# Kernel optimization log

Measured on AMD Instinct MI355X. Metric: run time of the kernel, lower is better.

## Reference

```python
import jax, jax.numpy as jnp
import numpy as np

N = 50000
E = 800000
F_IN = 128
H = 64
C = 10
BN_EPS = 1e-5


def _glorot(key, shape):
    fan_in = shape[0]
    return jax.random.normal(key, shape, dtype=jnp.float32) / jnp.sqrt(jnp.float32(fan_in))


def setup_inputs() -> dict:
    key = jax.random.key(0)
    ks = jax.random.split(key, 16)
    inp = {
        "x": jax.random.normal(ks[0], (N, F_IN), dtype=jnp.float32),
        "edge_index": jax.random.randint(ks[1], (2, E), 0, N, dtype=jnp.int64),
    }
    # GINConv layer params: eps (train_eps=True, init 0), 2-layer MLP, BN affine
    dims = [(F_IN, H), (H, H), (H, H)]
    for i, (din, dout) in enumerate(dims, start=1):
        k1, k2 = jax.random.split(ks[1 + i], 2)
        inp[f"eps{i}"] = jnp.float32(0.0)
        inp[f"w{i}a"] = _glorot(k1, (din, H))
        inp[f"b{i}a"] = jnp.zeros((H,), jnp.float32)
        inp[f"w{i}b"] = _glorot(k2, (H, H))
        inp[f"b{i}b"] = jnp.zeros((H,), jnp.float32)
        inp[f"g{i}"] = jnp.ones((H,), jnp.float32)
        inp[f"be{i}"] = jnp.zeros((H,), jnp.float32)
    inp["lin_w"] = _glorot(ks[10], (H, C))
    inp["lin_b"] = jnp.zeros((C,), jnp.float32)
    return inp


def _gin_conv(x, src, dst, eps, wa, ba, wb, bb, g, be):
    # sum-aggregate neighbor features: scatter-add x[src] into dst rows
    agg = jax.ops.segment_sum(x[src], dst, num_segments=N)
    h = (1.0 + eps) * x + agg
    # MLP: Linear-ReLU-Linear-ReLU-BatchNorm1d (training-mode batch stats)
    h = jax.nn.relu(h @ wa + ba)
    h = jax.nn.relu(h @ wb + bb)
    mean = jnp.mean(h, axis=0)
    var = jnp.var(h, axis=0)
    return (h - mean) * jax.lax.rsqrt(var + BN_EPS) * g + be


def reference(x, edge_index,
              eps1, w1a, b1a, w1b, b1b, g1, be1,
              eps2, w2a, b2a, w2b, b2b, g2, be2,
              eps3, w3a, b3a, w3b, b3b, g3, be3,
              lin_w, lin_b):
    src, dst = edge_index[0], edge_index[1]
    h = jax.nn.relu(_gin_conv(x, src, dst, eps1, w1a, b1a, w1b, b1b, g1, be1))
    h = jax.nn.relu(_gin_conv(h, src, dst, eps2, w2a, b2a, w2b, b2b, g2, be2))
    h = jax.nn.relu(_gin_conv(h, src, dst, eps3, w3a, b3a, w3b, b3b, g3, be3))
    return h @ lin_w + lin_b
```

## Files before the change

kernel.cpp:

```cpp
#include <hip/hip_runtime.h>
#include <hip/hip_fp16.h>

#define NN 50000
#define NGROUP 3125
#define NCHUNK 391
#define CHCAP 3072
#define SLAB 2048
#define BN_EPS 1e-5f

typedef unsigned int uint;
typedef unsigned short ushort;
typedef _Float16 half8 __attribute__((ext_vector_type(8)));
typedef _Float16 half2t __attribute__((ext_vector_type(2)));
typedef float floatx4 __attribute__((ext_vector_type(4)));

__device__ __forceinline__ int aswz(int slot) { return slot ^ ((slot >> 4) & 7); }

__device__ __forceinline__ float h_lo(uint u) {
    return __half2float(__ushort_as_half((ushort)(u & 0xFFFFu)));
}
__device__ __forceinline__ float h_hi(uint u) {
    return __half2float(__ushort_as_half((ushort)(u >> 16)));
}
__device__ __forceinline__ void unpack8(uint4 v, float* f) {
    f[0] = h_lo(v.x); f[1] = h_hi(v.x);
    f[2] = h_lo(v.y); f[3] = h_hi(v.y);
    f[4] = h_lo(v.z); f[5] = h_hi(v.z);
    f[6] = h_lo(v.w); f[7] = h_hi(v.w);
}
__device__ __forceinline__ uint pkadd(uint a, uint b) {
    half2t x = __builtin_bit_cast(half2t, a);
    half2t y = __builtin_bit_cast(half2t, b);
    half2t r = x + y;
    return __builtin_bit_cast(uint, r);
}

__global__ __launch_bounds__(256, 4) void sortA_kernel(
    const int* __restrict__ ei, int* __restrict__ gcur,
    uint* __restrict__ bucket, int E)
{
    __shared__ int s_hist[NCHUNK];
    __shared__ int s_offs[NCHUNK];
    __shared__ int s_cur[NCHUNK];
    __shared__ int s_gb[NCHUNK];
    __shared__ int s_scanA[512], s_scanB[512];
    __shared__ uint s_sorted[SLAB];

    const int tid  = threadIdx.x;
    const int base = blockIdx.x * SLAB;
    const int cnt  = min(SLAB, E - base);

    for (int i = tid; i < NCHUNK; i += 256) s_hist[i] = 0;
    __syncthreads();
    for (int i = tid; i < cnt; i += 256) {
        int dst = ei[E + base + i];
        atomicAdd(&s_hist[dst >> 7], 1);
    }
    __syncthreads();
    for (int i = tid; i < 512; i += 256) s_scanA[i] = (i < NCHUNK) ? s_hist[i] : 0;
    __syncthreads();
    int* sa = s_scanA; int* sb = s_scanB;
    for (int off = 1; off < 512; off <<= 1) {
        for (int i = tid; i < 512; i += 256)
            sb[i] = sa[i] + ((i >= off) ? sa[i - off] : 0);
        __syncthreads();
        int* t = sa; sa = sb; sb = t;
    }
    for (int i = tid; i < NCHUNK; i += 256) {
        int excl = sa[i] - s_hist[i];
        s_offs[i] = excl;
        s_cur[i]  = excl;
    }
    __syncthreads();
    for (int i = tid; i < cnt; i += 256) {
        int src = ei[base + i];
        int dst = ei[E + base + i];
        int c = dst >> 7;
        uint v = (uint)src | ((uint)(dst & 127) << 16) | ((uint)c << 23);
        int pos = atomicAdd(&s_cur[c], 1);
        s_sorted[pos] = v;
    }
    __syncthreads();
    for (int c = tid; c < NCHUNK; c += 256) {
        int n = s_hist[c];
        s_gb[c] = n ? atomicAdd(&gcur[c], n) : 0;
    }
    __syncthreads();
    for (int i = tid; i < cnt; i += 256) {
        uint v = s_sorted[i];
        int c = v >> 23;
        int li = i - s_offs[c];
        bucket[(size_t)c * CHCAP + s_gb[c] + li] = v;
    }
}

__global__ __launch_bounds__(256) void fillB_kernel(
    const uint* __restrict__ bucket, const int* __restrict__ gcur,
    int* __restrict__ rowPtr, int* __restrict__ csr_src)
{
    __shared__ int s_hist[128];
    __shared__ int s_excl[128];
    __shared__ int s_cur[128];
    __shared__ int s_ws[4];
    __shared__ int s_base;
    const int c = blockIdx.x;
    const int tid = threadIdx.x;
    const int cnt = gcur[c];
    const int row0 = c * 128;

    int part = 0;
    for (int i = tid; i < c; i += 256) part += gcur[i];
    #pragma unroll
    for (int off = 32; off >= 1; off >>= 1) part += __shfl_down(part, off, 64);
    if ((tid & 63) == 0) s_ws[tid >> 6] = part;
    if (tid < 128) s_hist[tid] = 0;
    __syncthreads();
    if (tid == 0) s_base = s_ws[0] + s_ws[1] + s_ws[2] + s_ws[3];
    __syncthreads();
    const int base = s_base;
    if (tid == 0 && c == NCHUNK - 1) rowPtr[NN] = base + cnt;

    for (int i = tid; i < cnt; i += 256) {
        uint v = bucket[(size_t)c * CHCAP + i];
        atomicAdd(&s_hist[(v >> 16) & 127], 1);
    }
    __syncthreads();
    if (tid < 128) {
        int lane = tid & 63;
        int v = s_hist[tid];
        int incl = v;
        #pragma unroll
        for (int off = 1; off < 64; off <<= 1) {
            int t = __shfl_up(incl, off, 64);
            if (lane >= off) incl += t;
        }
        s_excl[tid] = incl - v;
    }
    __syncthreads();
    if (tid < 128) {
        int excl = s_excl[tid];
        if (tid >= 64) excl += s_excl[63] + s_hist[63];
        s_cur[tid] = excl;
        int row = row0 + tid;
        if (row < NN) rowPtr[row] = base + excl;
    }
    __syncthreads();
    for (int i = tid; i < cnt; i += 256) {
        uint v = bucket[(size_t)c * CHCAP + i];
        int dl  = (v >> 16) & 127;
        int src = v & 0xFFFFu;
        int ofs = atomicAdd(&s_cur[dl], 1);
        csr_src[base + ofs] = src;
    }
}

template<int FIN, bool APPLY>
__global__ __launch_bounds__(256, 4) void proj_kernel(
    const void* __restrict__ in_v,
    const float* __restrict__ stats_in, const float* __restrict__ g_in,
    const float* __restrict__ be_in,
    const float* __restrict__ wa,
    ushort* __restrict__ y_out)
{
    constexpr int KC = FIN / 32;
    __shared__ __align__(16) _Float16 s_B[FIN * 64];
    __shared__ __align__(16) _Float16 s_Y[4][1024];

    const int tid = threadIdx.x, w = tid >> 6, lane = tid & 63;
    const int q = lane >> 4, mm = lane & 15;

    for (int i = tid; i < FIN * 64; i += 256) {
        int j = i & 7, l = (i >> 3) & 63, t = i >> 9;
        int kc = t >> 2, nt = t & 3;
        int k = kc * 32 + (l >> 4) * 8 + j;
        int n = nt * 16 + (l & 15);
        s_B[i] = (_Float16)wa[k * 64 + n];
    }

    float scv[2][8], shv[2][8];
    if (APPLY) {
        #pragma unroll
        for (int kc = 0; kc < 2; kc++)
            #pragma unroll
            for (int j = 0; j < 8; j++) {
                int c = kc * 32 + q * 8 + j;
                float mean = stats_in[c] * (1.0f / NN);
                float var  = stats_in[64 + c] * (1.0f / NN) - mean * mean;
                float rstd = rsqrtf(var + BN_EPS);
                float s    = rstd * g_in[c];
                scv[kc][j] = s;
                shv[kc][j] = be_in[c] - mean * s;
            }
    }
    __syncthreads();

    int g = blockIdx.x * 4 + w;
    if (g >= NGROUP) return;
    const int row = g * 16 + mm;

    half8 af[KC];
    if (FIN == 128) {
        const float* xin = (const float*)in_v;
        #pragma unroll
        for (int kc = 0; kc < KC; kc++) {
            const float* p = xin + (size_t)row * 128 + kc * 32 + q * 8;
            float4 a = *(const float4*)p;
            float4 b = *(const float4*)(p + 4);
            half8 hv;
            hv[0] = (_Float16)a.x; hv[1] = (_Float16)a.y;
            hv[2] = (_Float16)a.z; hv[3] = (_Float16)a.w;
            hv[4] = (_Float16)b.x; hv[5] = (_Float16)b.y;
            hv[6] = (_Float16)b.z; hv[7] = (_Float16)b.w;
            af[kc] = hv;
        }
    } else {
        const ushort* hin = (const ushort*)in_v;
        #pragma unroll
        for (int kc = 0; kc < KC; kc++) {
            uint4 vv = *(const uint4*)(hin + (size_t)row * 64 + kc * 32 + q * 8);
            float f[8]; unpack8(vv, f);
            half8 hv;
            #pragma unroll
            for (int j = 0; j < 8; j++) {
                float z = APPLY ? fmaxf(fmaf(f[j], scv[kc][j], shv[kc][j]), 0.0f) : f[j];
                hv[j] = (_Float16)z;
            }
            af[kc] = hv;
        }
    }

    floatx4 acc[4] = {};
    #pragma unroll
    for (int nt = 0; nt < 4; nt++)
        #pragma unroll
        for (int kc = 0; kc < KC; kc++) {
            half8 bf = *(const half8*)(s_B + ((size_t)(kc * 4 + nt) * 64 + lane) * 8);
            acc[nt] = __builtin_amdgcn_mfma_f32_16x16x32_f16(af[kc], bf, acc[nt], 0, 0, 0);
        }

    _Float16* s_Yw = &s_Y[w][0];
    #pragma unroll
    for (int nt = 0; nt < 4; nt++)
        #pragma unroll
        for (int r = 0; r < 4; r++)
            s_Yw[(q * 4 + r) * 64 + nt * 16 + mm] = (_Float16)acc[nt][r];
    half8 t0 = *(const half8*)(s_Yw + lane * 8);
    half8 t1 = *(const half8*)(s_Yw + 512 + lane * 8);
    half8* dst = (half8*)((_Float16*)y_out + (size_t)g * 1024);
    dst[lane] = t0;
    dst[64 + lane] = t1;
}

__global__ __launch_bounds__(512, 5) void gin_gather_kernel(
    const ushort* __restrict__ y,
    const int* __restrict__ rowPtr, const int* __restrict__ csr_src,
    const float* __restrict__ eps_p, const float* __restrict__ ba,
    const float* __restrict__ wb, const float* __restrict__ bb,
    ushort* __restrict__ h_out, float* __restrict__ stats_out)
{
    __shared__ __align__(16) _Float16 s_B2[64 * 64];
    __shared__ __align__(16) _Float16 s_A[2][1024];
    __shared__ float s_red[2][128];

    const int tid = threadIdx.x, w = tid >> 6, lane = tid & 63;
    const int gl = w >> 2;
    const int m  = (w & 3) * 4;
    const int cc = lane & 7, gph = lane >> 3;
    const int q = lane >> 4, mm = lane & 15;

    for (int i = tid; i < 64 * 64; i += 512) {
        int j = i & 7, l = (i >> 3) & 63, t = i >> 9;
        int kc = t >> 2, nt = t & 3;
        int k = kc * 32 + (l >> 4) * 8 + j;
        int n = nt * 16 + (l & 15);
        s_B2[i] = (_Float16)wb[k * 64 + n];
    }
    if (tid < 256) ((float*)s_red)[tid] = 0.0f;

    const float eps1 = 1.0f + eps_p[0];
    __syncthreads();

    const uint4* y4 = (const uint4*)y;
    const int g = blockIdx.x * 2 + gl;

    if (g < NGROUP) {
        const int row0 = g * 16;
        _Float16* s_Aw = &s_A[gl][0];

        int e[4], en[4], s[4];
        uint4 v[4];
        uint4 pk[4];
        #pragma unroll
        for (int i = 0; i < 4; i++) {
            int row = row0 + m + i;
            e[i] = rowPtr[row] + gph;
            en[i] = rowPtr[row + 1];
            pk[i].x = pk[i].y = pk[i].z = pk[i].w = 0u;
        }
        #pragma unroll
        for (int i = 0; i < 4; i++) s[i] = (e[i] < en[i]) ? csr_src[e[i]] : -1;
        #pragma unroll
        for (int i = 0; i < 4; i++) if (s[i] >= 0) v[i] = y4[(size_t)s[i] * 8 + cc];

        int mx = max(max(s[0], s[1]), max(s[2], s[3]));
        while (mx >= 0) {
            int n[4]; uint4 p[4];
            #pragma unroll
            for (int i = 0; i < 4; i++) {
                n[i] = -1;
                if (s[i] >= 0) { e[i] += 8; n[i] = (e[i] < en[i]) ? csr_src[e[i]] : -1; }
            }
            #pragma unroll
            for (int i = 0; i < 4; i++) if (n[i] >= 0) p[i] = y4[(size_t)n[i] * 8 + cc];
            #pragma unroll
            for (int i = 0; i < 4; i++) {
                if (s[i] >= 0) {
                    pk[i].x = pkadd(pk[i].x, v[i].x);
                    pk[i].y = pkadd(pk[i].y, v[i].y);
                    pk[i].z = pkadd(pk[i].z, v[i].z);
                    pk[i].w = pkadd(pk[i].w, v[i].w);
                }
                s[i] = n[i]; v[i] = p[i];
            }
            mx = max(max(s[0], s[1]), max(s[2], s[3]));
        }

        #pragma unroll
        for (int i = 0; i < 4; i++) {
            float a[8];
            unpack8(pk[i], a);
            if (gph == 0) {
                uint4 sv = y4[(size_t)(row0 + m + i) * 8 + cc];
                float f[8]; unpack8(sv, f);
                #pragma unroll
                for (int j = 0; j < 8; j++) a[j] = fmaf(eps1, f[j], a[j]);
            }
            #pragma unroll
            for (int off = 8; off < 64; off <<= 1)
                #pragma unroll
                for (int j = 0; j < 8; j++)
                    a[j] += __shfl_xor(a[j], off, 64);
            if (gph == 0) {
                half8 hv;
                #pragma unroll
                for (int j = 0; j < 8; j++)
                    hv[j] = (_Float16)fmaxf(a[j] + ba[8 * cc + j], 0.0f);
                int slot = (cc >> 2) * 64 + (cc & 3) * 16 + (m + i);
                *(half8*)(s_Aw + (size_t)aswz(slot) * 8) = hv;
            }
        }
    }
    __syncthreads();

    if ((w & 3) == 0 && g < NGROUP) {
        const int row0 = g * 16;
        _Float16* s_Aw = &s_A[gl][0];
        float bbv[4];
        #pragma unroll
        for (int nt = 0; nt < 4; nt++) bbv[nt] = bb[nt * 16 + mm];

        half8 af2[2];
        #pragma unroll
        for (int kc = 0; kc < 2; kc++)
            af2[kc] = *(const half8*)(s_Aw + (size_t)aswz(kc * 64 + lane) * 8);
        floatx4 acc2[4] = {};
        #pragma unroll
        for (int nt = 0; nt < 4; nt++)
            #pragma unroll
            for (int kc = 0; kc < 2; kc++) {
                half8 bf = *(const half8*)(s_B2 + ((size_t)(kc * 4 + nt) * 64 + lane) * 8);
                acc2[nt] = __builtin_amdgcn_mfma_f32_16x16x32_f16(af2[kc], bf, acc2[nt], 0, 0, 0);
            }

        float bn_s[4] = {0.f, 0.f, 0.f, 0.f};
        float bn_q[4] = {0.f, 0.f, 0.f, 0.f};
        #pragma unroll
        for (int nt = 0; nt < 4; nt++)
            #pragma unroll
            for (int r = 0; r < 4; r++) {
                float val = fmaxf(acc2[nt][r] + bbv[nt], 0.0f);
                bn_s[nt] += val;
                bn_q[nt] += val * val;
                s_Aw[(q * 4 + r) * 64 + nt * 16 + mm] = (_Float16)val;
            }
        half8 t0 = *(const half8*)(s_Aw + lane * 8);
        half8 t1 = *(const half8*)(s_Aw + 512 + lane * 8);
        half8* dst = (half8*)((_Float16*)h_out + (size_t)row0 * 64);
        dst[lane] = t0;
        dst[64 + lane] = t1;

        #pragma unroll
        for (int nt = 0; nt < 4; nt++) {
            bn_s[nt] += __shfl_xor(bn_s[nt], 16, 64);
            bn_s[nt] += __shfl_xor(bn_s[nt], 32, 64);
            bn_q[nt] += __shfl_xor(bn_q[nt], 16, 64);
            bn_q[nt] += __shfl_xor(bn_q[nt], 32, 64);
        }
        if (lane < 16) {
            #pragma unroll
            for (int nt = 0; nt < 4; nt++) {
                s_red[gl][nt * 16 + lane]      = bn_s[nt];
                s_red[gl][64 + nt * 16 + lane] = bn_q[nt];
            }
        }
    }
    __syncthreads();
    if (w == 0) {
        atomicAdd(&stats_out[lane],      s_red[0][lane]      + s_red[1][lane]);
        atomicAdd(&stats_out[64 + lane], s_red[0][64 + lane] + s_red[1][64 + lane]);
    }
}

__global__ __launch_bounds__(256) void final_linear_kernel(
    const ushort* __restrict__ h, const float* __restrict__ stats,
    const float* __restrict__ g, const float* __restrict__ be,
    const float* __restrict__ w, const float* __restrict__ b,
    float* __restrict__ out)
{
    __shared__ float s_w[640];
    __shared__ float s_b[10];
    __shared__ float s_scale[64];
    __shared__ float s_shift[64];
    for (int i = threadIdx.x; i < 640; i += 256) s_w[i] = w[i];
    if (threadIdx.x < 10) s_b[threadIdx.x] = b[threadIdx.x];
    if (threadIdx.x < 64) {
        int c = threadIdx.x;
        float mean = stats[c] * (1.0f / NN);
        float var  = stats[64 + c] * (1.0f / NN) - mean * mean;
        float rstd = rsqrtf(var + BN_EPS);
        float s    = rstd * g[c];
        s_scale[c] = s;
        s_shift[c] = be[c] - mean * s;
    }
    __syncthreads();
    int row = blockIdx.x * 256 + threadIdx.x;
    if (row >= NN) return;
    float acc[10];
    #pragma unroll
    for (int c = 0; c < 10; c++) acc[c] = s_b[c];
    const uint4* hr = (const uint4*)(h + (size_t)row * 64);
    #pragma unroll
    for (int ch = 0; ch < 8; ch++) {
        uint4 v = hr[ch];
        float f[8]; unpack8(v, f);
        #pragma unroll
        for (int j = 0; j < 8; j++) {
            int k = ch * 8 + j;
            float val = fmaxf(fmaf(f[j], s_scale[k], s_shift[k]), 0.0f);
            #pragma unroll
            for (int c = 0; c < 10; c++) acc[c] = fmaf(val, s_w[k * 10 + c], acc[c]);
        }
    }
    #pragma unroll
    for (int c = 0; c < 10; c++) out[row * 10 + c] = acc[c];
}

extern "C" void kernel_launch(void* const* d_in, const int* in_sizes, int n_in,
                              void* d_out, int out_size, void* d_ws, size_t ws_size,
                              hipStream_t stream)
{
    const float* x  = (const float*)d_in[0];
    const int*   ei = (const int*)d_in[1];
    const int E = in_sizes[1] / 2;

    const float* eps[3]; const float* wa[3]; const float* ba[3];
    const float* wb[3];  const float* bb[3]; const float* g[3]; const float* be[3];
    for (int i = 0; i < 3; i++) {
        int base = 2 + 7 * i;
        eps[i] = (const float*)d_in[base + 0];
        wa[i]  = (const float*)d_in[base + 1];
        ba[i]  = (const float*)d_in[base + 2];
        wb[i]  = (const float*)d_in[base + 3];
        bb[i]  = (const float*)d_in[base + 4];
        g[i]   = (const float*)d_in[base + 5];
        be[i]  = (const float*)d_in[base + 6];
    }
    const float* lin_w = (const float*)d_in[23];
    const float* lin_b = (const float*)d_in[24];
    float* out = (float*)d_out;

    char*  base   = (char*)d_ws;
    int*   gcur   = (int*)base;
    float* stats  = (float*)(gcur + 512);
    int*   rowPtr = (int*)(stats + 384);
    uint*  bucket = (uint*)(rowPtr + NN + 1);
    int*   csrsrc = (int*)(bucket + (size_t)NCHUNK * CHCAP);
    size_t ioff   = (char*)(csrsrc + E) - base;
    ushort* yb    = (ushort*)(base + ((ioff + 15) & ~(size_t)15));
    ushort* hA    = yb + (size_t)NN * 64;
    ushort* hB    = hA + (size_t)NN * 64;

    const int SB = (E + SLAB - 1) / SLAB;
    const int PB = (NGROUP + 3) / 4;
    const int GB = (NGROUP + 1) / 2;

    hipMemsetAsync(gcur, 0, (512 + 384) * sizeof(int), stream);
    sortA_kernel<<<SB, 256, 0, stream>>>(ei, gcur, bucket, E);
    fillB_kernel<<<NCHUNK, 256, 0, stream>>>(bucket, gcur, rowPtr, csrsrc);

    proj_kernel<128, false><<<PB, 256, 0, stream>>>(
        x, nullptr, nullptr, nullptr, wa[0], yb);
    gin_gather_kernel<<<GB, 512, 0, stream>>>(
        yb, rowPtr, csrsrc, eps[0], ba[0], wb[0], bb[0], hA, stats);
    proj_kernel<64, true><<<PB, 256, 0, stream>>>(
        hA, stats, g[0], be[0], wa[1], yb);
    gin_gather_kernel<<<GB, 512, 0, stream>>>(
        yb, rowPtr, csrsrc, eps[1], ba[1], wb[1], bb[1], hB, stats + 128);
    proj_kernel<64, true><<<PB, 256, 0, stream>>>(
        hB, stats + 128, g[1], be[1], wa[2], yb);
    gin_gather_kernel<<<GB, 512, 0, stream>>>(
        yb, rowPtr, csrsrc, eps[2], ba[2], wb[2], bb[2], hA, stats + 256);
    final_linear_kernel<<<(NN + 255) / 256, 256, 0, stream>>>(
        hA, stats + 256, g[2], be[2], lin_w, lin_b, out);
}
```

Baseline: 370.1 us.

## Precompute fp16 swizzled wb in proj kernel and replicate BN stat accumulators

The second-layer weight is now converted and swizzled to fp16 once, by the first eight blocks of the projection kernel, into a workspace buffer. The gather kernel then loads it with a single vector copy per thread instead of recomputing the conversion in every block. BN statistics atomics are spread over eight replicated accumulators keyed by block index, which cuts atomic contention, and consumers sum the replicas. The gather kernel's launch-bounds occupancy hint is also lowered from 5 to 4. This adds a small amount of work to the proj kernel and a larger memset.

```diff
diff --git a/kernel.cpp b/kernel.cpp
--- a/kernel.cpp
+++ b/kernel.cpp
@@ -6,6 +6,7 @@
 #define NCHUNK 391
 #define CHCAP 3072
 #define SLAB 2048
+#define NREP 8
 #define BN_EPS 1e-5f
 
 typedef unsigned int uint;
@@ -160,6 +161,7 @@
     const float* __restrict__ stats_in, const float* __restrict__ g_in,
     const float* __restrict__ be_in,
     const float* __restrict__ wa,
+    const float* __restrict__ wb_src, _Float16* __restrict__ wbh_out,
     ushort* __restrict__ y_out)
 {
     constexpr int KC = FIN / 32;
@@ -168,6 +170,17 @@
 
     const int tid = threadIdx.x, w = tid >> 6, lane = tid & 63;
     const int q = lane >> 4, mm = lane & 15;
+
+    if (blockIdx.x < 8) {
+        for (int t = tid; t < 512; t += 256) {
+            int i = blockIdx.x * 512 + t;
+            int j = i & 7, l = (i >> 3) & 63, tt = i >> 9;
+            int kc = tt >> 2, nt = tt & 3;
+            int k = kc * 32 + (l >> 4) * 8 + j;
+            int n = nt * 16 + (l & 15);
+            wbh_out[i] = (_Float16)wb_src[k * 64 + n];
+        }
+    }
 
     for (int i = tid; i < FIN * 64; i += 256) {
         int j = i & 7, l = (i >> 3) & 63, t = i >> 9;
@@ -184,8 +197,14 @@
             #pragma unroll
             for (int j = 0; j < 8; j++) {
                 int c = kc * 32 + q * 8 + j;
-                float mean = stats_in[c] * (1.0f / NN);
-                float var  = stats_in[64 + c] * (1.0f / NN) - mean * mean;
+                float s0 = 0.f, s1 = 0.f;
+                #pragma unroll
+                for (int r = 0; r < NREP; r++) {
+                    s0 += stats_in[r * 128 + c];
+                    s1 += stats_in[r * 128 + 64 + c];
+                }
+                float mean = s0 * (1.0f / NN);
+                float var  = s1 * (1.0f / NN) - mean * mean;
                 float rstd = rsqrtf(var + BN_EPS);
                 float s    = rstd * g_in[c];
                 scv[kc][j] = s;
@@ -251,11 +270,11 @@
     dst[64 + lane] = t1;
 }
 
-__global__ __launch_bounds__(512, 5) void gin_gather_kernel(
+__global__ __launch_bounds__(512, 4) void gin_gather_kernel(
     const ushort* __restrict__ y,
     const int* __restrict__ rowPtr, const int* __restrict__ csr_src,
     const float* __restrict__ eps_p, const float* __restrict__ ba,
-    const float* __restrict__ wb, const float* __restrict__ bb,
+    const _Float16* __restrict__ wbh, const float* __restrict__ bb,
     ushort* __restrict__ h_out, float* __restrict__ stats_out)
 {
     __shared__ __align__(16) _Float16 s_B2[64 * 64];
@@ -268,13 +287,7 @@
     const int cc = lane & 7, gph = lane >> 3;
     const int q = lane >> 4, mm = lane & 15;
 
-    for (int i = tid; i < 64 * 64; i += 512) {
-        int j = i & 7, l = (i >> 3) & 63, t = i >> 9;
-        int kc = t >> 2, nt = t & 3;
-        int k = kc * 32 + (l >> 4) * 8 + j;
-        int n = nt * 16 + (l & 15);
-        s_B2[i] = (_Float16)wb[k * 64 + n];
-    }
+    ((half8*)s_B2)[tid] = ((const half8*)wbh)[tid];
     if (tid < 256) ((float*)s_red)[tid] = 0.0f;
 
     const float eps1 = 1.0f + eps_p[0];
@@ -406,8 +419,9 @@
     }
     __syncthreads();
     if (w == 0) {
-        atomicAdd(&stats_out[lane],      s_red[0][lane]      + s_red[1][lane]);
-        atomicAdd(&stats_out[64 + lane], s_red[0][64 + lane] + s_red[1][64 + lane]);
+        float* srep = stats_out + (size_t)(blockIdx.x & (NREP - 1)) * 128;
+        atomicAdd(&srep[lane],      s_red[0][lane]      + s_red[1][lane]);
+        atomicAdd(&srep[64 + lane], s_red[0][64 + lane] + s_red[1][64 + lane]);
     }
 }
 
@@ -425,8 +439,14 @@
     if (threadIdx.x < 10) s_b[threadIdx.x] = b[threadIdx.x];
     if (threadIdx.x < 64) {
         int c = threadIdx.x;
-        float mean = stats[c] * (1.0f / NN);
-        float var  = stats[64 + c] * (1.0f / NN) - mean * mean;
+        float s0 = 0.f, s1 = 0.f;
+        #pragma unroll
+        for (int r = 0; r < NREP; r++) {
+            s0 += stats[r * 128 + c];
+            s1 += stats[r * 128 + 64 + c];
+        }
+        float mean = s0 * (1.0f / NN);
+        float var  = s1 * (1.0f / NN) - mean * mean;
         float rstd = rsqrtf(var + BN_EPS);
         float s    = rstd * g[c];
         s_scale[c] = s;
@@ -482,11 +502,12 @@
     char*  base   = (char*)d_ws;
     int*   gcur   = (int*)base;
     float* stats  = (float*)(gcur + 512);
-    int*   rowPtr = (int*)(stats + 384);
+    int*   rowPtr = (int*)(stats + 3 * NREP * 128);
     uint*  bucket = (uint*)(rowPtr + NN + 1);
     int*   csrsrc = (int*)(bucket + (size_t)NCHUNK * CHCAP);
-    size_t ioff   = (char*)(csrsrc + E) - base;
-    ushort* yb    = (ushort*)(base + ((ioff + 15) & ~(size_t)15));
+    size_t hoff   = (char*)(csrsrc + E) - base;
+    _Float16* wbh = (_Float16*)(base + ((hoff + 15) & ~(size_t)15));
+    ushort* yb    = (ushort*)(wbh + 4096);
     ushort* hA    = yb + (size_t)NN * 64;
     ushort* hB    = hA + (size_t)NN * 64;
 
@@ -494,22 +515,22 @@
     const int PB = (NGROUP + 3) / 4;
     const int GB = (NGROUP + 1) / 2;
 
-    hipMemsetAsync(gcur, 0, (512 + 384) * sizeof(int), stream);
+    hipMemsetAsync(gcur, 0, (512 + 3 * NREP * 128) * sizeof(int), stream);
     sortA_kernel<<<SB, 256, 0, stream>>>(ei, gcur, bucket, E);
     fillB_kernel<<<NCHUNK, 256, 0, stream>>>(bucket, gcur, rowPtr, csrsrc);
 
     proj_kernel<128, false><<<PB, 256, 0, stream>>>(
-        x, nullptr, nullptr, nullptr, wa[0], yb);
+        x, nullptr, nullptr, nullptr, wa[0], wb[0], wbh, yb);
     gin_gather_kernel<<<GB, 512, 0, stream>>>(
-        yb, rowPtr, csrsrc, eps[0], ba[0], wb[0], bb[0], hA, stats);
+        yb, rowPtr, csrsrc, eps[0], ba[0], wbh, bb[0], hA, stats);
     proj_kernel<64, true><<<PB, 256, 0, stream>>>(
-        hA, stats, g[0], be[0], wa[1], yb);
+        hA, stats, g[0], be[0], wa[1], wb[1], wbh, yb);
     gin_gather_kernel<<<GB, 512, 0, stream>>>(
-        yb, rowPtr, csrsrc, eps[1], ba[1], wb[1], bb[1], hB, stats + 128);
+        yb, rowPtr, csrsrc, eps[1], ba[1], wbh, bb[1], hB, stats + NREP * 128);
     proj_kernel<64, true><<<PB, 256, 0, stream>>>(
-        hB, stats + 128, g[1], be[1], wa[2], yb);
+        hB, stats + NREP * 128, g[1], be[1], wa[2], wb[2], wbh, yb);
     gin_gather_kernel<<<GB, 512, 0, stream>>>(
-        yb, rowPtr, csrsrc, eps[2], ba[2], wb[2], bb[2], hA, stats + 256);
+        yb, rowPtr, csrsrc, eps[2], ba[2], wbh, bb[2], hA, stats + 2 * NREP * 128);
     final_linear_kernel<<<(NN + 255) / 256, 256, 0, stream>>>(
-        hA, stats + 256, g[2], be[2], lin_w, lin_b, out);
-}
+        hA, stats + 2 * NREP * 128, g[2], be[2], lin_w, lin_b, out);
+}
```

Result: faster. 325.1 us (-12.2%).
